# Kernel optimization log

Measured on AMD Instinct MI355X. Metric: run time of the kernel, lower is better.

## Reference

```python
import jax, jax.numpy as jnp
from jax import lax
import numpy as np

B, H, W = 8, 352, 1216
CLIPVARIANCE = 5.0   # init kwarg
MAXRANGE = 32        # init kwarg

# 1-pixel shifts with zero padding. out[...,m,n] = x at the shifted location.
def s_pos_w(x):  # out[..., n] = x[..., n-1]
    return jnp.pad(x[..., :, :-1], ((0, 0), (0, 0), (0, 0), (1, 0)))

def s_neg_w(x):  # out[..., n] = x[..., n+1]
    return jnp.pad(x[..., :, 1:], ((0, 0), (0, 0), (0, 0), (0, 1)))

def s_pos_h(x):  # out[..., m, :] = x[..., m-1, :]
    return jnp.pad(x[..., :-1, :], ((0, 0), (0, 0), (1, 0), (0, 0)))

def s_neg_h(x):  # out[..., m, :] = x[..., m+1, :]
    return jnp.pad(x[..., 1:, :], ((0, 0), (0, 0), (0, 1), (0, 0)))


def _dir_accumulate(shift, logstep, depthin, maskf, var_d):
    """Scan outward up to MAXRANGE steps in one direction, accumulating
    confidence weights exp(-min(var, clip)) and variance-weighted depth
    hypotheses depth[src] * exp(integrated log-gradient along the path).
    Paths break at the first unmasked pixel (valid is a running product)."""
    z = jnp.zeros_like(depthin)

    def body(carry, _):
        valid, c, dsh, vsh, aw, awd = carry
        valid = shift(valid * maskf)          # path contiguity
        c = logstep(c)                         # integrated log-depth ratio
        dsh = shift(dsh)                       # source-pixel depth
        vsh = shift(vsh)                       # source-pixel variance
        w = jnp.exp(-jnp.minimum(vsh, CLIPVARIANCE)) * valid
        aw = aw + w
        awd = awd + w * jnp.exp(c) * dsh
        return (valid, c, dsh, vsh, aw, awd), None

    init = (jnp.ones_like(depthin), z, depthin, var_d, z, z)
    (_, _, _, _, aw, awd), _ = lax.scan(body, init, None, length=MAXRANGE)
    return aw, awd


def crf_lateralre(pred_log, mask, variance, depthin):
    """One 4-direction variance-weighted CRF integration pass."""
    maskf = mask.astype(depthin.dtype)
    plog_h = pred_log[:, 0:1]  # log d[m,n+1] - log d[m,n]
    plog_v = pred_log[:, 1:2]  # log d[m+1,n] - log d[m,n]

    dirs = [
        (s_pos_w, lambda c: s_pos_w(c + plog_h), variance[:, 0:1]),  # from left
        (s_neg_w, lambda c: s_neg_w(c) - plog_h, variance[:, 1:2]),  # from right
        (s_pos_h, lambda c: s_pos_h(c + plog_v), variance[:, 2:3]),  # from above
        (s_neg_h, lambda c: s_neg_h(c) - plog_v, variance[:, 3:4]),  # from below
    ]

    tot_w = jnp.zeros_like(depthin)
    tot_wd = jnp.zeros_like(depthin)
    for shift, logstep, var_d in dirs:
        aw, awd = _dir_accumulate(shift, logstep, depthin, maskf, var_d)
        tot_w = tot_w + aw
        tot_wd = tot_wd + awd

    lateralre = jnp.where(tot_w > 0, tot_wd / jnp.maximum(tot_w, 1e-12), 0.0)
    return lateralre * maskf


def setup_inputs() -> dict:
    key = jax.random.key(0)
    k1, k2, k3, k4 = jax.random.split(key, 4)
    pred_log = jax.random.normal(k1, (B, 2, H, W), jnp.float32) * 0.05
    mask = (jax.random.uniform(k2, (B, 1, H, W)) < 0.9).astype(jnp.int32)
    variance = jax.random.uniform(k3, (B, 4, H, W), jnp.float32) * 8.0
    depthin = jax.random.uniform(k4, (B, 1, H, W), jnp.float32) * 10.0 + 1.0
    lam = jnp.array([0.2], jnp.float32)
    return {"pred_log": pred_log, "mask": mask, "variance": variance,
            "depthin": depthin, "lam": lam, "times": 1}


def reference(pred_log, mask, variance, depthin, lam, times):
    depthout = depthin
    for _ in range(times):
        lateralre = crf_lateralre(pred_log, mask, variance, depthout)
        sel = (lateralre > 0).astype(depthin.dtype)
        depthout = (1 - sel) * depthin + sel * (depthin * (1 - lam) + lateralre * lam)
    return depthout
```

## Files before the change

kernel.cpp:

```cpp
#include <hip/hip_runtime.h>

#define HH 352
#define WW 1216
#define HW (HH*WW)
#define BB 8
#define CLIPV 5.0f
#define MAXR 32

#define VR 22
#define NBAND (HH/VR)
#define PFD 6

__global__ __launch_bounds__(128, 4) void crf_vert(
    const float* __restrict__ pred_log, const int* __restrict__ mask,
    const float* __restrict__ variance, const float* __restrict__ depth,
    float* __restrict__ vw, float* __restrict__ vwd)
{
    __shared__ float2 obuf[2][VR][64];

    const int lane = threadIdx.x & 63;
    const int dir  = threadIdx.x >> 6;

    const int id   = blockIdx.x;
    const int xcd  = id & 7;
    const int seq  = id >> 3;
    const int wc   = seq % 19;
    const int t2   = seq / 19;
    const int band = xcd * 2 + (t2 & 1);
    const int b    = t2 >> 1;

    const int w    = wc * 64 + lane;

    const float* plog_v = pred_log + ((size_t)b*2 + 1) * HW;
    const int*   m  = mask     + (size_t)b*HW;
    const float* vp = variance + ((size_t)b*4 + (dir ? 3 : 2)) * HW;
    const float* d  = depth    + (size_t)b*HW;

    const int h0 = band * VR;
    const int h1 = h0 + VR;

    int   pm[PFD]; float ppl[PFD], pvv[PFD], pdd[PFD];
    float rq_q[VR], rq_w[VR];

    if (dir == 0) {
        const int hs = h0 - MAXR;
        #pragma unroll
        for (int p = 0; p < PFD; ++p) {
            int h = hs + p;
            int hc = min(max(h, 0), HH-1);
            int idx = hc * WW + w;
            pm[p]  = (h >= 0) ? m[idx] : 0;
            ppl[p] = plog_v[idx];
            pvv[p] = vp[idx];
            pdd[p] = d[idx];
        }
        float Q = 0.f, W = 0.f, EA = 1.f;
        int last_inv = hs - 1;
        #pragma unroll
        for (int it = 0; it < VR + MAXR; ++it) {
            const int h = hs + it;
            const int sl = it % PFD;
            int   mi = pm[sl];
            float pl = ppl[sl], vvx = pvv[sl], dd = pdd[sl];
            {
                int hp = h + PFD;
                int hc = min(max(hp, 0), HH-1);
                int idx = hc * WW + w;
                pm[sl]  = (hp >= 0 && hp < HH) ? m[idx] : 0;
                ppl[sl] = plog_v[idx];
                pvv[sl] = vp[idx];
                pdd[sl] = d[idx];
            }
            if (it >= MAXR) obuf[0][it - MAXR][lane] = make_float2(W, EA * Q);
            bool  res = (mi == 0);
            float g   = __expf(pl);
            float wt  = __expf(-fminf(vvx, CLIPV));
            float q   = wt * dd * __builtin_amdgcn_rcpf(EA);
            q  = res ? 0.f : q;
            wt = res ? 0.f : wt;
            Q  = res ? 0.f : (Q + q);
            W  = res ? 0.f : (W + wt);
            EA = res ? 1.f : (EA * g);
            last_inv = res ? h : last_inv;
            if (it < VR) { rq_q[it] = q; rq_w[it] = wt; }
            if (it >= MAXR) {
                bool alive = (h - MAXR) > last_inv;
                Q -= alive ? rq_q[it - MAXR] : 0.f;
                W -= alive ? rq_w[it - MAXR] : 0.f;
            }
        }
    } else {
        const int hs = h1 - 1 + MAXR;
        #pragma unroll
        for (int p = 0; p < PFD; ++p) {
            int h = hs - p;
            int hc = min(max(h, 0), HH-1);
            int idx = hc * WW + w;
            pm[p]  = (h < HH) ? m[idx] : 0;
            ppl[p] = plog_v[idx];
            pvv[p] = vp[idx];
            pdd[p] = d[idx];
        }
        float Q = 0.f, W = 0.f, ED = 1.f;
        int last_inv = hs + 1;
        #pragma unroll
        for (int it = 0; it < VR + MAXR; ++it) {
            const int h = hs - it;
            const int sl = it % PFD;
            int   mi = pm[sl];
            float pl = ppl[sl], vvx = pvv[sl], dd = pdd[sl];
            {
                int hp = h - PFD;
                int hc = min(max(hp, 0), HH-1);
                int idx = hc * WW + w;
                pm[sl]  = (hp >= 0 && hp < HH) ? m[idx] : 0;
                ppl[sl] = plog_v[idx];
                pvv[sl] = vp[idx];
                pdd[sl] = d[idx];
            }
            float g   = __expf(pl);
            float EDh = ED * g;
            if (it >= MAXR) obuf[1][VR - 1 - (it - MAXR)][lane] = make_float2(W, Q * __builtin_amdgcn_rcpf(EDh));
            bool  res = (mi == 0);
            float wt  = __expf(-fminf(vvx, CLIPV));
            float q   = wt * dd * EDh;
            q  = res ? 0.f : q;
            wt = res ? 0.f : wt;
            Q  = res ? 0.f : (Q + q);
            W  = res ? 0.f : (W + wt);
            ED = res ? 1.f : EDh;
            last_inv = res ? h : last_inv;
            if (it < VR) { rq_q[it] = q; rq_w[it] = wt; }
            if (it >= MAXR) {
                bool alive = (h + MAXR) < last_inv;
                Q -= alive ? rq_q[it - MAXR] : 0.f;
                W -= alive ? rq_w[it - MAXR] : 0.f;
            }
        }
    }
    __syncthreads();
    float* pvw  = vw  + (size_t)b*HW;
    float* pvwd = vwd + (size_t)b*HW;
    const int w0 = wc * 64;
    #pragma unroll
    for (int k = 0; k < VR*64; k += 128) {
        int kk = k + threadIdx.x;
        int r = kk >> 6, l = kk & 63;
        float2 a = obuf[0][r][l], c = obuf[1][r][l];
        int idx = (h0 + r) * WW + w0 + l;
        pvw [idx] = a.x + c.x;
        pvwd[idx] = a.y + c.y;
    }
}


__global__ __launch_bounds__(256) void crf_horiz(
    const float* __restrict__ pred_log, const int* __restrict__ mask,
    const float* __restrict__ variance, const float* __restrict__ depth,
    const float* __restrict__ lam_p,
    const float* __restrict__ vw, const float* __restrict__ vwd,
    float* __restrict__ out)
{
    __shared__ float sG[WW];
    __shared__ float sH[WW];
    __shared__ float sI[WW];
    __shared__ float sJ[WW];
    __shared__ float sEt[19], sEti[19], sTw0[19], sTq0[19];
    __shared__ unsigned long long sBal[19];

    const int tid  = threadIdx.x;
    const int lane = tid & 63;
    const int wv   = tid >> 6;
    const int i    = blockIdx.x;
    const int h    = (i & 7) * 44 + (i >> 3);
    const int b    = blockIdx.y;

    const float* plrow = pred_log + (size_t)b*2*HW + h*WW;
    const int*   mrow  = mask     + (size_t)b*HW   + h*WW;
    const float* v0row = variance + (size_t)b*4*HW + h*WW;
    const float* v1row = v0row + HW;
    const float* drow  = depth    + (size_t)b*HW   + h*WW;
    const float* vwrow = vw  + (size_t)b*HW + h*WW;
    const float* vwdrow= vwd + (size_t)b*HW + h*WW;
    float*       orow  = out + (size_t)b*HW + h*WW;

    float l_pAx[5], l_xw0[5], l_xq0[5], l_iw1[5], l_iq1[5], l_m[5], l_d[5];

    #pragma unroll
    for (int r = 0; r < 5; ++r) {
        int c = r*4 + wv;
        if (c < 19) {
            int j = c*64 + lane;
            float pl  = plrow[j];
            int   mi  = mrow[j];
            float dj  = drow[j];
            float wt0 = __expf(-fminf(v0row[j], CLIPV));
            float wt1 = __expf(-fminf(v1row[j], CLIPV));
            float ipA = pl;
            #pragma unroll
            for (int dlt = 1; dlt < 64; dlt <<= 1) {
                float u = __shfl_up(ipA, dlt, 64);
                if (lane >= dlt) ipA += u;
            }
            float pAx = ipA - pl;
            float S   = __shfl(ipA, 63, 64);
            float Einv = __expf(-pAx);
            float q0 = wt0 * dj * Einv;
            float q1 = wt1 * dj * Einv;
            float iw0 = wt0, iq0 = q0, iw1 = wt1, iq1 = q1;
            #pragma unroll
            for (int dlt = 1; dlt < 64; dlt <<= 1) {
                float a = __shfl_up(iw0, dlt, 64);
                float e = __shfl_up(iq0, dlt, 64);
                float f = __shfl_up(iw1, dlt, 64);
                float g = __shfl_up(iq1, dlt, 64);
                if (lane >= dlt) { iw0 += a; iq0 += e; iw1 += f; iq1 += g; }
            }
            sG[j] = iw0 - wt0;
            sH[j] = iq0 - q0;
            sI[j] = iw1;
            sJ[j] = iq1;
            unsigned long long bal = __ballot(mi == 0);
            if (lane == 63) {
                sEt[c]  = __expf(S);
                sEti[c] = __expf(-S);
                sTw0[c] = iw0;
                sTq0[c] = iq0;
            }
            if (lane == 0) sBal[c] = bal;
            l_pAx[r] = pAx; l_xw0[r] = iw0 - wt0; l_xq0[r] = iq0 - q0;
            l_iw1[r] = iw1; l_iq1[r] = iq1;
            l_m[r] = (float)mi; l_d[r] = dj;
        }
    }
    __syncthreads();

    const float lam = lam_p[0];

    #pragma unroll
    for (int r = 0; r < 5; ++r) {
        int c = r*4 + wv;
        if (c < 19) {
            const int c0 = c*64;
            const int j  = c0 + lane;
            float E = __expf(l_pAx[r]);
            unsigned long long balOwn = sBal[c];
            unsigned long long mb = balOwn & ((1ull << lane) - 1ull);
            int lm = mb ? (c0 + 63 - __builtin_clzll(mb)) : -1;
            if (c > 0 && lane < 32) {
                unsigned long long mp = sBal[c-1] & ~((1ull << (lane + 32)) - 1ull);
                if (mp) { int lm2 = c0 - 64 + 63 - __builtin_clzll(mp); lm = max(lm, lm2); }
            }
            int a0 = max(j - MAXR, lm + 1);
            float W0, Q0;
            if (a0 >= c0) {
                W0 = l_xw0[r] - sG[a0];
                Q0 = E * (l_xq0[r] - sH[a0]);
            } else {
                W0 = l_xw0[r] + (sTw0[c-1] - sG[a0]);
                Q0 = E * l_xq0[r] + E * sEt[c-1] * (sTq0[c-1] - sH[a0]);
            }
            int nm = 1 << 30;
            if (lane < 63) {
                unsigned long long nb = balOwn >> (lane + 1);
                if (nb) nm = j + 1 + __builtin_ctzll(nb);
            }
            if (c < 18 && lane >= 32) {
                unsigned long long nn = sBal[c+1] & ((1ull << (lane - 31)) - 1ull);
                if (nn) nm = min(nm, c0 + 64 + (int)__builtin_ctzll(nn));
            }
            int b1 = min(j + MAXR, nm - 1);
            b1 = min(b1, WW - 1);
            int endin = min(b1, c0 + 63);
            float W1 = 0.f, Q1 = 0.f;
            if (endin > j) {
                W1 = sI[endin] - l_iw1[r];
                Q1 = E * (sJ[endin] - l_iq1[r]);
            }
            if (b1 > c0 + 63) {
                W1 += sI[b1];
                Q1 += E * sEti[c] * sJ[b1];
            }
            float totw  = W0 + W1 + vwrow[j];
            float totwd = Q0 + Q1 + vwdrow[j];
            float lat = (totw > 0.f) ? (totwd / fmaxf(totw, 1e-12f)) : 0.f;
            lat *= l_m[r];
            float dj = l_d[r];
            orow[j] = (lat > 0.f) ? (dj * (1.f - lam) + lat * lam) : dj;
        }
    }
}

#define BWF 256
#define PADF 32
#define LWF (BWF + 2*PADF)

__global__ __launch_bounds__(256) void crf_fallback(
    const float* __restrict__ pred_log, const int* __restrict__ mask,
    const float* __restrict__ variance, const float* __restrict__ depth,
    const float* __restrict__ lam_p, float* __restrict__ out)
{
    __shared__ float s_m[LWF], s_wt0[LWF], s_wt1[LWF], s_gh[LWF], s_ghi[LWF], s_d[LWF];
    const int t  = threadIdx.x;
    const int i  = blockIdx.x;
    const int h  = (i & 7) * 44 + (i >> 3);
    const int w0 = blockIdx.y * BWF;
    const int b  = blockIdx.z;
    const float* plog_h = pred_log + (size_t)b * 2 * HW;
    const float* plog_v = plog_h + HW;
    const int*   m      = mask   + (size_t)b * HW;
    const float* v0     = variance + (size_t)b * 4 * HW;
    const float* v1     = v0 + HW;
    const float* v2     = v0 + 2 * HW;
    const float* v3     = v0 + 3 * HW;
    const float* d      = depth + (size_t)b * HW;
    for (int j = t; j < LWF; j += BWF) {
        int gw = w0 - PADF + j;
        float mf=0.f, wt0=0.f, wt1=0.f, gh=1.f, ghi=1.f, dd=0.f;
        if (gw >= 0 && gw < WW) {
            int idx = h * WW + gw;
            mf = (float)m[idx];
            float pl = plog_h[idx];
            gh = __expf(pl); ghi = __expf(-pl);
            wt0 = __expf(-fminf(v0[idx], CLIPV));
            wt1 = __expf(-fminf(v1[idx], CLIPV));
            dd = d[idx];
        }
        s_m[j]=mf; s_wt0[j]=wt0; s_wt1[j]=wt1; s_gh[j]=gh; s_ghi[j]=ghi; s_d[j]=dd;
    }
    __syncthreads();
    const int w = w0 + t;
    if (w >= WW) return;
    const int c = t + PADF;
    float totw = 0.f, totwd = 0.f;
    { float e=1.f, valid=1.f;
      #pragma unroll 8
      for (int k=1;k<=MAXR;++k){int s=c-k; valid*=s_m[s]; e*=s_gh[s];
        float wgt=s_wt0[s]*valid; totw+=wgt; totwd+=wgt*e*s_d[s];} }
    { float e=1.f, valid=1.f;
      #pragma unroll 8
      for (int k=1;k<=MAXR;++k){int s=c+k; e*=s_ghi[s-1]; valid*=s_m[s];
        float wgt=s_wt1[s]*valid; totw+=wgt; totwd+=wgt*e*s_d[s];} }
    { const int kup=min(MAXR,h); float e=1.f, valid=1.f;
      #pragma unroll 4
      for (int k=1;k<=kup;++k){int idx=(h-k)*WW+w; valid*=(float)m[idx];
        e*=__expf(plog_v[idx]); float wgt=__expf(-fminf(v2[idx],CLIPV))*valid;
        totw+=wgt; totwd+=wgt*e*d[idx];} }
    { const int kdn=min(MAXR,HH-1-h); float e=1.f, valid=1.f;
      #pragma unroll 4
      for (int k=1;k<=kdn;++k){int idx=(h+k)*WW+w; e*=__expf(-plog_v[idx-WW]);
        valid*=(float)m[idx]; float wgt=__expf(-fminf(v3[idx],CLIPV))*valid;
        totw+=wgt; totwd+=wgt*e*d[idx];} }
    const int base = h * WW + w;
    float lat = (totw > 0.f) ? (totwd / fmaxf(totw, 1e-12f)) : 0.f;
    lat *= s_m[c];
    float lam = lam_p[0];
    float di  = s_d[c];
    out[(size_t)b * HW + base] = (lat > 0.f) ? (di * (1.f - lam) + lat * lam) : di;
}

extern "C" void kernel_launch(void* const* d_in, const int* in_sizes, int n_in,
                              void* d_out, int out_size, void* d_ws, size_t ws_size,
                              hipStream_t stream) {
    const float* pred_log = (const float*)d_in[0];
    const int*   mask     = (const int*)  d_in[1];
    const float* variance = (const float*)d_in[2];
    const float* depthin  = (const float*)d_in[3];
    const float* lam      = (const float*)d_in[4];
    float* out = (float*)d_out;

    const size_t need = 2ull * BB * HW * sizeof(float);
    if (ws_size >= need) {
        float* vw  = (float*)d_ws;
        float* vwd = vw + (size_t)BB * HW;
        dim3 vgrid(19 * NBAND * BB, 1, 1);
        hipLaunchKernelGGL(crf_vert, vgrid, dim3(128), 0, stream,
                           pred_log, mask, variance, depthin, vw, vwd);
        dim3 hgrid(HH, BB);
        hipLaunchKernelGGL(crf_horiz, hgrid, dim3(256), 0, stream,
                           pred_log, mask, variance, depthin, lam, vw, vwd, out);
    } else {
        dim3 fgrid(HH, (WW + BWF - 1) / BWF, BB);
        hipLaunchKernelGGL(crf_fallback, fgrid, dim3(BWF), 0, stream,
                           pred_log, mask, variance, depthin, lam, out);
    }
}
```

Before: 198.4 us.

## Split vertical pass into per-direction 64-thread blocks writing separate float2 buffers

Adds a new vertical kernel where each direction (top-down, bottom-up) runs as its own 64-thread block and writes (W, Q) float2 results straight to global memory, with no shared-memory staging or block barrier. The horizontal kernel now reads and sums the two per-direction buffers itself. The prefetch depth goes from 6 to 8, so the slot index becomes a bitmask. This doubles block-level parallelism and removes the sync between the two directions, at the cost of twice the workspace and extra global write and read traffic. The new path runs only when the workspace is large enough; otherwise the old path is kept.

```diff
diff --git a/kernel.cpp b/kernel.cpp
--- a/kernel.cpp
+++ b/kernel.cpp
@@ -9,26 +9,22 @@
 
 #define VR 22
 #define NBAND (HH/VR)
-#define PFD 6
-
-__global__ __launch_bounds__(128, 4) void crf_vert(
+#define PFD 8
+
+__global__ __launch_bounds__(64) void crf_vert_s(
     const float* __restrict__ pred_log, const int* __restrict__ mask,
     const float* __restrict__ variance, const float* __restrict__ depth,
-    float* __restrict__ vw, float* __restrict__ vwd)
+    float2* __restrict__ vq0, float2* __restrict__ vq1)
 {
-    __shared__ float2 obuf[2][VR][64];
-
-    const int lane = threadIdx.x & 63;
-    const int dir  = threadIdx.x >> 6;
-
+    const int lane = threadIdx.x;
     const int id   = blockIdx.x;
     const int xcd  = id & 7;
     const int seq  = id >> 3;
     const int wc   = seq % 19;
-    const int t2   = seq / 19;
-    const int band = xcd * 2 + (t2 & 1);
-    const int b    = t2 >> 1;
-
+    const int r    = seq / 19;
+    const int dir  = r & 1;
+    const int band = xcd * 2 + ((r >> 1) & 1);
+    const int b    = r >> 2;
     const int w    = wc * 64 + lane;
 
     const float* plog_v = pred_log + ((size_t)b*2 + 1) * HW;
@@ -43,6 +39,7 @@
     float rq_q[VR], rq_w[VR];
 
     if (dir == 0) {
+        float2* oq = vq0 + (size_t)b*HW;
         const int hs = h0 - MAXR;
         #pragma unroll
         for (int p = 0; p < PFD; ++p) {
@@ -59,7 +56,7 @@
         #pragma unroll
         for (int it = 0; it < VR + MAXR; ++it) {
             const int h = hs + it;
-            const int sl = it % PFD;
+            const int sl = it & (PFD-1);
             int   mi = pm[sl];
             float pl = ppl[sl], vvx = pvv[sl], dd = pdd[sl];
             {
@@ -71,7 +68,7 @@
                 pvv[sl] = vp[idx];
                 pdd[sl] = d[idx];
             }
-            if (it >= MAXR) obuf[0][it - MAXR][lane] = make_float2(W, EA * Q);
+            if (it >= MAXR) oq[h * WW + w] = make_float2(W, EA * Q);
             bool  res = (mi == 0);
             float g   = __expf(pl);
             float wt  = __expf(-fminf(vvx, CLIPV));
@@ -90,6 +87,7 @@
             }
         }
     } else {
+        float2* oq = vq1 + (size_t)b*HW;
         const int hs = h1 - 1 + MAXR;
         #pragma unroll
         for (int p = 0; p < PFD; ++p) {
@@ -106,7 +104,7 @@
         #pragma unroll
         for (int it = 0; it < VR + MAXR; ++it) {
             const int h = hs - it;
-            const int sl = it % PFD;
+            const int sl = it & (PFD-1);
             int   mi = pm[sl];
             float pl = ppl[sl], vvx = pvv[sl], dd = pdd[sl];
             {
@@ -120,7 +118,7 @@
             }
             float g   = __expf(pl);
             float EDh = ED * g;
-            if (it >= MAXR) obuf[1][VR - 1 - (it - MAXR)][lane] = make_float2(W, Q * __builtin_amdgcn_rcpf(EDh));
+            if (it >= MAXR) oq[h * WW + w] = make_float2(W, Q * __builtin_amdgcn_rcpf(EDh));
             bool  res = (mi == 0);
             float wt  = __expf(-fminf(vvx, CLIPV));
             float q   = wt * dd * EDh;
@@ -138,6 +136,119 @@
             }
         }
     }
+}
+
+__global__ __launch_bounds__(128, 4) void crf_vert(
+    const float* __restrict__ pred_log, const int* __restrict__ mask,
+    const float* __restrict__ variance, const float* __restrict__ depth,
+    float* __restrict__ vw, float* __restrict__ vwd)
+{
+    __shared__ float2 obuf[2][VR][64];
+    const int lane = threadIdx.x & 63;
+    const int dir  = threadIdx.x >> 6;
+    const int id   = blockIdx.x;
+    const int xcd  = id & 7;
+    const int seq  = id >> 3;
+    const int wc   = seq % 19;
+    const int t2   = seq / 19;
+    const int band = xcd * 2 + (t2 & 1);
+    const int b    = t2 >> 1;
+    const int w    = wc * 64 + lane;
+
+    const float* plog_v = pred_log + ((size_t)b*2 + 1) * HW;
+    const int*   m  = mask     + (size_t)b*HW;
+    const float* vp = variance + ((size_t)b*4 + (dir ? 3 : 2)) * HW;
+    const float* d  = depth    + (size_t)b*HW;
+    const int h0 = band * VR;
+    const int h1 = h0 + VR;
+
+    int   pm[PFD]; float ppl[PFD], pvv[PFD], pdd[PFD];
+    float rq_q[VR], rq_w[VR];
+
+    if (dir == 0) {
+        const int hs = h0 - MAXR;
+        #pragma unroll
+        for (int p = 0; p < PFD; ++p) {
+            int h = hs + p;
+            int hc = min(max(h, 0), HH-1);
+            int idx = hc * WW + w;
+            pm[p]  = (h >= 0) ? m[idx] : 0;
+            ppl[p] = plog_v[idx]; pvv[p] = vp[idx]; pdd[p] = d[idx];
+        }
+        float Q = 0.f, W = 0.f, EA = 1.f;
+        int last_inv = hs - 1;
+        #pragma unroll
+        for (int it = 0; it < VR + MAXR; ++it) {
+            const int h = hs + it;
+            const int sl = it & (PFD-1);
+            int   mi = pm[sl];
+            float pl = ppl[sl], vvx = pvv[sl], dd = pdd[sl];
+            {
+                int hp = h + PFD;
+                int hc = min(max(hp, 0), HH-1);
+                int idx = hc * WW + w;
+                pm[sl]  = (hp >= 0 && hp < HH) ? m[idx] : 0;
+                ppl[sl] = plog_v[idx]; pvv[sl] = vp[idx]; pdd[sl] = d[idx];
+            }
+            if (it >= MAXR) obuf[0][it - MAXR][lane] = make_float2(W, EA * Q);
+            bool  res = (mi == 0);
+            float g   = __expf(pl);
+            float wt  = __expf(-fminf(vvx, CLIPV));
+            float q   = wt * dd * __builtin_amdgcn_rcpf(EA);
+            q  = res ? 0.f : q; wt = res ? 0.f : wt;
+            Q  = res ? 0.f : (Q + q); W = res ? 0.f : (W + wt);
+            EA = res ? 1.f : (EA * g);
+            last_inv = res ? h : last_inv;
+            if (it < VR) { rq_q[it] = q; rq_w[it] = wt; }
+            if (it >= MAXR) {
+                bool alive = (h - MAXR) > last_inv;
+                Q -= alive ? rq_q[it - MAXR] : 0.f;
+                W -= alive ? rq_w[it - MAXR] : 0.f;
+            }
+        }
+    } else {
+        const int hs = h1 - 1 + MAXR;
+        #pragma unroll
+        for (int p = 0; p < PFD; ++p) {
+            int h = hs - p;
+            int hc = min(max(h, 0), HH-1);
+            int idx = hc * WW + w;
+            pm[p]  = (h < HH) ? m[idx] : 0;
+            ppl[p] = plog_v[idx]; pvv[p] = vp[idx]; pdd[p] = d[idx];
+        }
+        float Q = 0.f, W = 0.f, ED = 1.f;
+        int last_inv = hs + 1;
+        #pragma unroll
+        for (int it = 0; it < VR + MAXR; ++it) {
+            const int h = hs - it;
+            const int sl = it & (PFD-1);
+            int   mi = pm[sl];
+            float pl = ppl[sl], vvx = pvv[sl], dd = pdd[sl];
+            {
+                int hp = h - PFD;
+                int hc = min(max(hp, 0), HH-1);
+                int idx = hc * WW + w;
+                pm[sl]  = (hp >= 0 && hp < HH) ? m[idx] : 0;
+                ppl[sl] = plog_v[idx]; pvv[sl] = vp[idx]; pdd[sl] = d[idx];
+            }
+            float g   = __expf(pl);
+            float EDh = ED * g;
+            if (it >= MAXR) obuf[1][VR - 1 - (it - MAXR)][lane] = make_float2(W, Q * __builtin_amdgcn_rcpf(EDh));
+            bool  res = (mi == 0);
+            float wt  = __expf(-fminf(vvx, CLIPV));
+            float q   = wt * dd * EDh;
+            q  = res ? 0.f : q; wt = res ? 0.f : wt;
+            Q  = res ? 0.f : (Q + q); W = res ? 0.f : (W + wt);
+            ED = res ? 1.f : EDh;
+            last_inv = res ? h : last_inv;
+            if (it < VR) { rq_q[it] = q; rq_w[it] = wt; }
+            if (it >= MAXR) {
+                bool alive = (h + MAXR) < last_inv;
+                Q -= alive ? rq_q[it - MAXR] : 0.f;
+                W -= alive ? rq_w[it - MAXR] : 0.f;
+            }
+        }
+    }
     __syncthreads();
     float* pvw  = vw  + (size_t)b*HW;
     float* pvwd = vwd + (size_t)b*HW;
@@ -145,20 +256,21 @@
     #pragma unroll
     for (int k = 0; k < VR*64; k += 128) {
         int kk = k + threadIdx.x;
-        int r = kk >> 6, l = kk & 63;
-        float2 a = obuf[0][r][l], c = obuf[1][r][l];
-        int idx = (h0 + r) * WW + w0 + l;
+        int rr = kk >> 6, l = kk & 63;
+        float2 a = obuf[0][rr][l], c = obuf[1][rr][l];
+        int idx = (h0 + rr) * WW + w0 + l;
         pvw [idx] = a.x + c.x;
         pvwd[idx] = a.y + c.y;
     }
 }
-
 
 __global__ __launch_bounds__(256) void crf_horiz(
     const float* __restrict__ pred_log, const int* __restrict__ mask,
     const float* __restrict__ variance, const float* __restrict__ depth,
     const float* __restrict__ lam_p,
     const float* __restrict__ vw, const float* __restrict__ vwd,
+    const float2* __restrict__ vq0, const float2* __restrict__ vq1,
+    const int wsmode,
     float* __restrict__ out)
 {
     __shared__ float sG[WW];
@@ -180,8 +292,10 @@
     const float* v0row = variance + (size_t)b*4*HW + h*WW;
     const float* v1row = v0row + HW;
     const float* drow  = depth    + (size_t)b*HW   + h*WW;
-    const float* vwrow = vw  + (size_t)b*HW + h*WW;
-    const float* vwdrow= vwd + (size_t)b*HW + h*WW;
+    const float*  vwrow = vw  + (size_t)b*HW + h*WW;
+    const float*  vwdrow= vwd + (size_t)b*HW + h*WW;
+    const float2* vq0row= vq0 + (size_t)b*HW + h*WW;
+    const float2* vq1row= vq1 + (size_t)b*HW + h*WW;
     float*       orow  = out + (size_t)b*HW + h*WW;
 
     float l_pAx[5], l_xw0[5], l_xq0[5], l_iw1[5], l_iq1[5], l_m[5], l_d[5];
@@ -281,8 +395,15 @@
                 W1 += sI[b1];
                 Q1 += E * sEti[c] * sJ[b1];
             }
-            float totw  = W0 + W1 + vwrow[j];
-            float totwd = Q0 + Q1 + vwdrow[j];
+            float vtw, vtwd;
+            if (wsmode) {
+                float2 a = vq0row[j], cc = vq1row[j];
+                vtw = a.x + cc.x; vtwd = a.y + cc.y;
+            } else {
+                vtw = vwrow[j]; vtwd = vwdrow[j];
+            }
+            float totw  = W0 + W1 + vtw;
+            float totwd = Q0 + Q1 + vtwd;
             float lat = (totw > 0.f) ? (totwd / fmaxf(totw, 1e-12f)) : 0.f;
             lat *= l_m[r];
             float dj = l_d[r];
@@ -369,8 +490,20 @@
     const float* lam      = (const float*)d_in[4];
     float* out = (float*)d_out;
 
-    const size_t need = 2ull * BB * HW * sizeof(float);
-    if (ws_size >= need) {
+    const size_t need4 = 2ull * BB * HW * sizeof(float2);
+    const size_t need2 = 2ull * BB * HW * sizeof(float);
+    if (ws_size >= need4) {
+        float2* vq0 = (float2*)d_ws;
+        float2* vq1 = vq0 + (size_t)BB * HW;
+        dim3 vgrid(19 * 2 * 2 * 8 * 8, 1, 1);
+        hipLaunchKernelGGL(crf_vert_s, vgrid, dim3(64), 0, stream,
+                           pred_log, mask, variance, depthin, vq0, vq1);
+        dim3 hgrid(HH, BB);
+        hipLaunchKernelGGL(crf_horiz, hgrid, dim3(256), 0, stream,
+                           pred_log, mask, variance, depthin, lam,
+                           (const float*)nullptr, (const float*)nullptr,
+                           vq0, vq1, 1, out);
+    } else if (ws_size >= need2) {
         float* vw  = (float*)d_ws;
         float* vwd = vw + (size_t)BB * HW;
         dim3 vgrid(19 * NBAND * BB, 1, 1);
@@ -378,7 +511,8 @@
                            pred_log, mask, variance, depthin, vw, vwd);
         dim3 hgrid(HH, BB);
         hipLaunchKernelGGL(crf_horiz, hgrid, dim3(256), 0, stream,
-                           pred_log, mask, variance, depthin, lam, vw, vwd, out);
+                           pred_log, mask, variance, depthin, lam,
+                           vw, vwd, (const float2*)nullptr, (const float2*)nullptr, 0, out);
     } else {
         dim3 fgrid(HH, (WW + BWF - 1) / BWF, BB);
         hipLaunchKernelGGL(crf_fallback, fgrid, dim3(BWF), 0, stream,
```

Result: slower. 207.3 us (+4.5%).

## Stream vertical scan inputs via async global-to-LDS ring and interleave workspace

Applied to the files above, without the earlier changes.

The vertical scan kernel now prefetches mask, log-gradient, variance and depth rows into a 12-slot LDS ring using global_load_lds async copies with a vmcnt wait, replacing the register prefetch arrays. The two direction branches are merged into one loop parameterised by step. The down-direction results stay in registers and are combined with the up-direction results from LDS, so only one wave writes. The vertical outputs are stored as an interleaved float2 workspace, read with one load in the horizontal kernel. This targets load latency and register pressure in the scan, at the risk of an incorrect hand-coded waitcnt, LDS traffic, and the removed occupancy hint.

```diff
diff --git a/kernel.cpp b/kernel.cpp
--- a/kernel.cpp
+++ b/kernel.cpp
@@ -1,4 +1,5 @@
 #include <hip/hip_runtime.h>
+#include <stdint.h>
 
 #define HH 352
 #define WW 1216
@@ -9,18 +10,30 @@
 
 #define VR 22
 #define NBAND (HH/VR)
-#define PFD 6
-
-__global__ __launch_bounds__(128, 4) void crf_vert(
+#define PFD 8
+#define SLOTS 12
+#define TOT (VR + MAXR)
+
+__device__ __forceinline__ void async_ld4(const void* g, void* l) {
+    __builtin_amdgcn_global_load_lds(
+        reinterpret_cast<const __attribute__((address_space(1))) uint32_t*>(
+            reinterpret_cast<uintptr_t>(g)),
+        reinterpret_cast<__attribute__((address_space(3))) uint32_t*>(
+            reinterpret_cast<uintptr_t>(l)),
+        4, 0, 0);
+}
+#define WAIT_VM28() __builtin_amdgcn_s_waitcnt(0x4F7C)
+
+__global__ __launch_bounds__(128) void crf_vert(
     const float* __restrict__ pred_log, const int* __restrict__ mask,
     const float* __restrict__ variance, const float* __restrict__ depth,
-    float* __restrict__ vw, float* __restrict__ vwd)
+    float2* __restrict__ vq)
 {
-    __shared__ float2 obuf[2][VR][64];
+    __shared__ float ring[2][SLOTS][4][64];
+    __shared__ float2 obuf0[VR][64];
 
     const int lane = threadIdx.x & 63;
     const int dir  = threadIdx.x >> 6;
-
     const int id   = blockIdx.x;
     const int xcd  = id & 7;
     const int seq  = id >> 3;
@@ -28,7 +41,6 @@
     const int t2   = seq / 19;
     const int band = xcd * 2 + (t2 & 1);
     const int b    = t2 >> 1;
-
     const int w    = wc * 64 + lane;
 
     const float* plog_v = pred_log + ((size_t)b*2 + 1) * HW;
@@ -38,127 +50,104 @@
 
     const int h0 = band * VR;
     const int h1 = h0 + VR;
-
-    int   pm[PFD]; float ppl[PFD], pvv[PFD], pdd[PFD];
+    const int hs   = dir ? (h1 - 1 + MAXR) : (h0 - MAXR);
+    const int step = dir ? -1 : 1;
+
     float rq_q[VR], rq_w[VR];
-
-    if (dir == 0) {
-        const int hs = h0 - MAXR;
-        #pragma unroll
-        for (int p = 0; p < PFD; ++p) {
-            int h = hs + p;
-            int hc = min(max(h, 0), HH-1);
+    float obw[VR], obq[VR];
+
+    #pragma unroll
+    for (int p = 0; p < PFD; ++p) {
+        int hp = hs + p * step;
+        int hc = min(max(hp, 0), HH-1);
+        int idx = hc * WW + w;
+        float* base = &ring[dir][p % SLOTS][0][0];
+        async_ld4(&m[idx],      base + 0*64 + lane);
+        async_ld4(&plog_v[idx], base + 1*64 + lane);
+        async_ld4(&vp[idx],     base + 2*64 + lane);
+        async_ld4(&d[idx],      base + 3*64 + lane);
+    }
+
+    float Q = 0.f, W = 0.f, EG = 1.f;
+    int last_inv = hs - step;
+
+    #pragma unroll
+    for (int it = 0; it < TOT; ++it) {
+        const int h  = hs + it * step;
+        const int sl = it % SLOTS;
+
+        WAIT_VM28();
+        const float* base = &ring[dir][sl][0][0];
+        int   mi  = ((unsigned)h < (unsigned)HH) ? __float_as_int(base[0*64 + lane]) : 0;
+        float pl  = base[1*64 + lane];
+        float vvx = base[2*64 + lane];
+        float dd  = base[3*64 + lane];
+
+        {
+            int hp = h + PFD * step;
+            int hc = min(max(hp, 0), HH-1);
             int idx = hc * WW + w;
-            pm[p]  = (h >= 0) ? m[idx] : 0;
-            ppl[p] = plog_v[idx];
-            pvv[p] = vp[idx];
-            pdd[p] = d[idx];
-        }
-        float Q = 0.f, W = 0.f, EA = 1.f;
-        int last_inv = hs - 1;
-        #pragma unroll
-        for (int it = 0; it < VR + MAXR; ++it) {
-            const int h = hs + it;
-            const int sl = it % PFD;
-            int   mi = pm[sl];
-            float pl = ppl[sl], vvx = pvv[sl], dd = pdd[sl];
-            {
-                int hp = h + PFD;
-                int hc = min(max(hp, 0), HH-1);
-                int idx = hc * WW + w;
-                pm[sl]  = (hp >= 0 && hp < HH) ? m[idx] : 0;
-                ppl[sl] = plog_v[idx];
-                pvv[sl] = vp[idx];
-                pdd[sl] = d[idx];
-            }
-            if (it >= MAXR) obuf[0][it - MAXR][lane] = make_float2(W, EA * Q);
-            bool  res = (mi == 0);
-            float g   = __expf(pl);
-            float wt  = __expf(-fminf(vvx, CLIPV));
-            float q   = wt * dd * __builtin_amdgcn_rcpf(EA);
+            float* nb = &ring[dir][(it + PFD) % SLOTS][0][0];
+            async_ld4(&m[idx],      nb + 0*64 + lane);
+            async_ld4(&plog_v[idx], nb + 1*64 + lane);
+            async_ld4(&vp[idx],     nb + 2*64 + lane);
+            async_ld4(&d[idx],      nb + 3*64 + lane);
+        }
+
+        bool  res = (mi == 0);
+        float g   = __expf(pl);
+        float wt  = __expf(-fminf(vvx, CLIPV));
+        float q, outw, outq;
+        if (dir == 0) {
+            outw = W; outq = EG * Q;
+            q = wt * dd * __builtin_amdgcn_rcpf(EG);
             q  = res ? 0.f : q;
             wt = res ? 0.f : wt;
             Q  = res ? 0.f : (Q + q);
             W  = res ? 0.f : (W + wt);
-            EA = res ? 1.f : (EA * g);
-            last_inv = res ? h : last_inv;
-            if (it < VR) { rq_q[it] = q; rq_w[it] = wt; }
-            if (it >= MAXR) {
-                bool alive = (h - MAXR) > last_inv;
-                Q -= alive ? rq_q[it - MAXR] : 0.f;
-                W -= alive ? rq_w[it - MAXR] : 0.f;
-            }
-        }
-    } else {
-        const int hs = h1 - 1 + MAXR;
-        #pragma unroll
-        for (int p = 0; p < PFD; ++p) {
-            int h = hs - p;
-            int hc = min(max(h, 0), HH-1);
-            int idx = hc * WW + w;
-            pm[p]  = (h < HH) ? m[idx] : 0;
-            ppl[p] = plog_v[idx];
-            pvv[p] = vp[idx];
-            pdd[p] = d[idx];
-        }
-        float Q = 0.f, W = 0.f, ED = 1.f;
-        int last_inv = hs + 1;
-        #pragma unroll
-        for (int it = 0; it < VR + MAXR; ++it) {
-            const int h = hs - it;
-            const int sl = it % PFD;
-            int   mi = pm[sl];
-            float pl = ppl[sl], vvx = pvv[sl], dd = pdd[sl];
-            {
-                int hp = h - PFD;
-                int hc = min(max(hp, 0), HH-1);
-                int idx = hc * WW + w;
-                pm[sl]  = (hp >= 0 && hp < HH) ? m[idx] : 0;
-                ppl[sl] = plog_v[idx];
-                pvv[sl] = vp[idx];
-                pdd[sl] = d[idx];
-            }
-            float g   = __expf(pl);
-            float EDh = ED * g;
-            if (it >= MAXR) obuf[1][VR - 1 - (it - MAXR)][lane] = make_float2(W, Q * __builtin_amdgcn_rcpf(EDh));
-            bool  res = (mi == 0);
-            float wt  = __expf(-fminf(vvx, CLIPV));
-            float q   = wt * dd * EDh;
+            EG = res ? 1.f : (EG * g);
+        } else {
+            float EDh = EG * g;
+            outw = W; outq = Q * __builtin_amdgcn_rcpf(EDh);
+            q = wt * dd * EDh;
             q  = res ? 0.f : q;
             wt = res ? 0.f : wt;
             Q  = res ? 0.f : (Q + q);
             W  = res ? 0.f : (W + wt);
-            ED = res ? 1.f : EDh;
-            last_inv = res ? h : last_inv;
-            if (it < VR) { rq_q[it] = q; rq_w[it] = wt; }
-            if (it >= MAXR) {
-                bool alive = (h + MAXR) < last_inv;
-                Q -= alive ? rq_q[it - MAXR] : 0.f;
-                W -= alive ? rq_w[it - MAXR] : 0.f;
-            }
-        }
-    }
+            EG = res ? 1.f : EDh;
+        }
+        last_inv = res ? h : last_inv;
+
+        if (it >= MAXR) {
+            if (dir == 0) obuf0[it - MAXR][lane] = make_float2(outw, outq);
+            else { obw[VR - 1 - (it - MAXR)] = outw; obq[VR - 1 - (it - MAXR)] = outq; }
+        }
+        if (it < VR) { rq_q[it] = q; rq_w[it] = wt; }
+        if (it >= MAXR) {
+            int s_out = h - MAXR * step;
+            bool alive = dir ? (s_out < last_inv) : (s_out > last_inv);
+            Q -= alive ? rq_q[it - MAXR] : 0.f;
+            W -= alive ? rq_w[it - MAXR] : 0.f;
+        }
+    }
+
     __syncthreads();
-    float* pvw  = vw  + (size_t)b*HW;
-    float* pvwd = vwd + (size_t)b*HW;
-    const int w0 = wc * 64;
-    #pragma unroll
-    for (int k = 0; k < VR*64; k += 128) {
-        int kk = k + threadIdx.x;
-        int r = kk >> 6, l = kk & 63;
-        float2 a = obuf[0][r][l], c = obuf[1][r][l];
-        int idx = (h0 + r) * WW + w0 + l;
-        pvw [idx] = a.x + c.x;
-        pvwd[idx] = a.y + c.y;
-    }
-}
-
+    if (dir == 1) {
+        float2* pvq = vq + (size_t)b*HW;
+        const int w0 = wc * 64;
+        #pragma unroll
+        for (int r = 0; r < VR; ++r) {
+            float2 a = obuf0[r][lane];
+            pvq[(h0 + r) * WW + w0 + lane] = make_float2(a.x + obw[r], a.y + obq[r]);
+        }
+    }
+}
 
 __global__ __launch_bounds__(256) void crf_horiz(
     const float* __restrict__ pred_log, const int* __restrict__ mask,
     const float* __restrict__ variance, const float* __restrict__ depth,
     const float* __restrict__ lam_p,
-    const float* __restrict__ vw, const float* __restrict__ vwd,
+    const float2* __restrict__ vq,
     float* __restrict__ out)
 {
     __shared__ float sG[WW];
@@ -180,8 +169,7 @@
     const float* v0row = variance + (size_t)b*4*HW + h*WW;
     const float* v1row = v0row + HW;
     const float* drow  = depth    + (size_t)b*HW   + h*WW;
-    const float* vwrow = vw  + (size_t)b*HW + h*WW;
-    const float* vwdrow= vwd + (size_t)b*HW + h*WW;
+    const float2* vqrow= vq  + (size_t)b*HW + h*WW;
     float*       orow  = out + (size_t)b*HW + h*WW;
 
     float l_pAx[5], l_xw0[5], l_xq0[5], l_iw1[5], l_iq1[5], l_m[5], l_d[5];
@@ -281,8 +269,9 @@
                 W1 += sI[b1];
                 Q1 += E * sEti[c] * sJ[b1];
             }
-            float totw  = W0 + W1 + vwrow[j];
-            float totwd = Q0 + Q1 + vwdrow[j];
+            float2 vt = vqrow[j];
+            float totw  = W0 + W1 + vt.x;
+            float totwd = Q0 + Q1 + vt.y;
             float lat = (totw > 0.f) ? (totwd / fmaxf(totw, 1e-12f)) : 0.f;
             lat *= l_m[r];
             float dj = l_d[r];
@@ -369,16 +358,15 @@
     const float* lam      = (const float*)d_in[4];
     float* out = (float*)d_out;
 
-    const size_t need = 2ull * BB * HW * sizeof(float);
+    const size_t need = (size_t)BB * HW * sizeof(float2);
     if (ws_size >= need) {
-        float* vw  = (float*)d_ws;
-        float* vwd = vw + (size_t)BB * HW;
+        float2* vq = (float2*)d_ws;
         dim3 vgrid(19 * NBAND * BB, 1, 1);
         hipLaunchKernelGGL(crf_vert, vgrid, dim3(128), 0, stream,
-                           pred_log, mask, variance, depthin, vw, vwd);
+                           pred_log, mask, variance, depthin, vq);
         dim3 hgrid(HH, BB);
         hipLaunchKernelGGL(crf_horiz, hgrid, dim3(256), 0, stream,
-                           pred_log, mask, variance, depthin, lam, vw, vwd, out);
+                           pred_log, mask, variance, depthin, lam, vq, out);
     } else {
         dim3 fgrid(HH, (WW + BWF - 1) / BWF, BB);
         hipLaunchKernelGGL(crf_fallback, fgrid, dim3(BWF), 0, stream,
```

Result: no change. 195.1 us (-1.7%).
